# Kernel tuning notes

Measured on AMD Instinct MI355X. Metric: run time of the kernel, lower is better.

The kernel has to match this reference:

```python
import jax, jax.numpy as jnp
import numpy as np

VOCAB = 32000
DIM = 1024
N = 4096
SMOOTHING = 0.1


def setup_inputs() -> dict:
    key = jax.random.key(0)
    kx, kw, ky = jax.random.split(key, 3)
    x = jax.random.normal(kx, (N, DIM), dtype=jnp.float32)
    # xavier_uniform for Linear(dim, vocab): bound = sqrt(6/(dim+vocab))
    bound = float(np.sqrt(6.0 / (DIM + VOCAB)))
    W = jax.random.uniform(kw, (VOCAB, DIM), dtype=jnp.float32, minval=-bound, maxval=bound)
    y = jax.random.randint(ky, (N,), 0, VOCAB, dtype=jnp.int64)
    return {"x": x, "W": W, "y": y}


def reference(x, W, y):
    # logits: [N, V]
    logits = jnp.einsum('nd,vd->nv', x, W)
    log_prb = jax.nn.log_softmax(logits, axis=-1)
    # nll_loss(log_prb, y) with mean reduction
    nll = -jnp.mean(jnp.take_along_axis(log_prb, y[:, None], axis=1)[:, 0])
    # label-smoothed loss: nll*(1-s) - mean(log_prb)*s  (mean over ALL N*V elems)
    loss = nll * (1.0 - SMOOTHING) - jnp.mean(log_prb) * SMOOTHING
    return loss
```

## Files before the change

### kernel.cpp

```cpp
#include <hip/hip_runtime.h>
#include <hip/hip_bf16.h>

#define N_TOK 4096
#define DIM   1024
#define VOCAB 32000
#define BM 128
#define BN 128
#define BKB 128
#define SMOOTH 0.1f

typedef __attribute__((ext_vector_type(4))) float float4v;
typedef __attribute__((ext_vector_type(2))) long long2v;

__global__ void cvt_fp8_2(const float* __restrict__ a, unsigned* __restrict__ da, int n8a,
                          const float* __restrict__ b, unsigned* __restrict__ db, int n8b) {
  int i = blockIdx.x * blockDim.x + threadIdx.x;
  const float4* s; uint2* d; int j; float scl;
  if (i < n8a)            { s = (const float4*)a; d = (uint2*)da; j = i;        scl = 1.f;  }
  else if (i < n8a + n8b) { s = (const float4*)b; d = (uint2*)db; j = i - n8a;  scl = 16.f; }
  else return;
  float4 v0 = s[j * 2], v1 = s[j * 2 + 1];
  unsigned lo = 0, hi = 0;
  lo = __builtin_amdgcn_cvt_pk_fp8_f32(v0.x * scl, v0.y * scl, lo, false);
  lo = __builtin_amdgcn_cvt_pk_fp8_f32(v0.z * scl, v0.w * scl, lo, true);
  hi = __builtin_amdgcn_cvt_pk_fp8_f32(v1.x * scl, v1.y * scl, hi, false);
  hi = __builtin_amdgcn_cvt_pk_fp8_f32(v1.z * scl, v1.w * scl, hi, true);
  uint2 o; o.x = lo; o.y = hi;
  d[j] = o;
}

__device__ __forceinline__ void gload_lds16(const void* g, void* l) {
  __builtin_amdgcn_global_load_lds((const __attribute__((address_space(1))) unsigned int*)g,
                                   (__attribute__((address_space(3))) unsigned int*)l,
                                   16, 0, 0);
}

__global__ __launch_bounds__(256)
void tgt_dot(const float* __restrict__ x, const float* __restrict__ W,
             const int* __restrict__ y, float* __restrict__ tgtRow) {
  const int n = blockIdx.x * 4 + (threadIdx.x >> 6);
  const int lane = threadIdx.x & 63;
  const float4* xr = (const float4*)(x + (size_t)n * DIM);
  const float4* wr = (const float4*)(W + (size_t)y[n] * DIM);
  float d = 0.f;
#pragma unroll
  for (int i = 0; i < 4; ++i) {
    float4 a = xr[lane + 64 * i], b = wr[lane + 64 * i];
    d += a.x * b.x + a.y * b.y + a.z * b.z + a.w * b.w;
  }
#pragma unroll
  for (int off = 32; off > 0; off >>= 1) d += __shfl_xor(d, off, 64);
  if (lane == 0) tgtRow[n] = d;
}

__global__ __launch_bounds__(256, 3)
void gemm_ce(const unsigned char* __restrict__ X8, const unsigned char* __restrict__ W8,
             float* __restrict__ rowExp, float* __restrict__ rowSum) {
  __shared__ __align__(16) unsigned char As[BM * BKB];
  __shared__ __align__(16) unsigned char Bs[BN * BKB];

  const int ib = blockIdx.x;
  const int jb = blockIdx.y;
  const int row0 = ib * BM;
  const int col0 = jb * BN;

  const int tid  = threadIdx.x;
  const int wv   = tid >> 6;
  const int lane = tid & 63;
  const int wr = wv >> 1, wc = wv & 1;
  const int quad = lane >> 4;
  const int r16  = lane & 15;
  const int lrow = lane >> 3;
  const int gcb  = (lane & 7) ^ (lrow & 7);
  const int r8   = r16 & 7;

  float4v acc[4][4];
#pragma unroll
  for (int i = 0; i < 4; ++i)
#pragma unroll
    for (int j = 0; j < 4; ++j) acc[i][j] = (float4v){0.f, 0.f, 0.f, 0.f};

  for (int kk = 0; kk < DIM; kk += BKB) {
    __syncthreads();
#pragma unroll
    for (int c = 0; c < 4; ++c) {
      const int rA = wv * 32 + c * 8;
      gload_lds16(X8 + (size_t)(row0 + rA + lrow) * DIM + kk + gcb * 16, &As[rA * BKB]);
      gload_lds16(W8 + (size_t)(col0 + rA + lrow) * DIM + kk + gcb * 16, &Bs[rA * BKB]);
    }
    __syncthreads();

#pragma unroll
    for (int rr = 0; rr < 2; ++rr) {
      const int cbOff = ((rr * 4 + quad) ^ r8) * 16;
      long2v bf[4];
#pragma unroll
      for (int j = 0; j < 4; ++j)
        bf[j] = *(const long2v*)&Bs[(wc * 64 + j * 16 + r16) * BKB + cbOff];
#pragma unroll
      for (int i = 0; i < 4; ++i) {
        const long2v af = *(const long2v*)&As[(wr * 64 + i * 16 + r16) * BKB + cbOff];
#pragma unroll
        for (int j = 0; j < 4; ++j) {
          acc[i][j] = __builtin_amdgcn_mfma_f32_16x16x32_fp8_fp8(af.x, bf[j].x, acc[i][j], 0, 0, 0);
          acc[i][j] = __builtin_amdgcn_mfma_f32_16x16x32_fp8_fp8(af.y, bf[j].y, acc[i][j], 0, 0, 0);
        }
      }
    }
  }

#pragma unroll
  for (int i = 0; i < 4; ++i)
#pragma unroll
    for (int r = 0; r < 4; ++r) {
      float se = 0.f, ss = 0.f;
#pragma unroll
      for (int j = 0; j < 4; ++j) {
        const float v = acc[i][j][r] * 0.0625f;
        ss += v;
        se += __expf(v);
      }
#pragma unroll
      for (int off = 1; off < 16; off <<= 1) {
        se += __shfl_xor(se, off, 64);
        ss += __shfl_xor(ss, off, 64);
      }
      if (r16 == 0) {
        const int rloc = wr * 64 + i * 16 + quad * 4 + r;
        atomicAdd(&rowExp[row0 + rloc], se);
        atomicAdd(&rowSum[row0 + rloc], ss);
      }
    }
}

__global__ void finalize_kernel(const float* __restrict__ rowExp, const float* __restrict__ rowSum,
                                const float* __restrict__ tgtRow, float* __restrict__ out) {
  __shared__ float s1[256], s2[256], s3[256];
  const int t = threadIdx.x;
  float a = 0.f, b = 0.f, c = 0.f;
  for (int n = t; n < N_TOK; n += 256) {
    a += logf(rowExp[n]);
    b += rowSum[n];
    c += tgtRow[n];
  }
  s1[t] = a; s2[t] = b; s3[t] = c;
  __syncthreads();
  for (int o = 128; o > 0; o >>= 1) {
    if (t < o) { s1[t] += s1[t + o]; s2[t] += s2[t + o]; s3[t] += s3[t + o]; }
    __syncthreads();
  }
  if (t == 0) {
    const float inviN = 1.0f / (float)N_TOK;
    out[0] = s1[0] * inviN
           - (1.0f - SMOOTH) * s3[0] * inviN
           - SMOOTH * s2[0] / ((float)N_TOK * (float)VOCAB);
  }
}

extern "C" void kernel_launch(void* const* d_in, const int* in_sizes, int n_in,
                              void* d_out, int out_size, void* d_ws, size_t ws_size,
                              hipStream_t stream) {
  const float* x = (const float*)d_in[0];
  const float* W = (const float*)d_in[1];
  const int*   y = (const int*)d_in[2];
  float* out = (float*)d_out;

  char* ws = (char*)d_ws;
  float* rowExp = (float*)(ws);
  float* rowSum = (float*)(ws + 16384);
  float* tgtRow = (float*)(ws + 32768);
  unsigned char* X8 = (unsigned char*)(ws + 65536);
  unsigned char* W8 = (unsigned char*)(ws + 65536 + (size_t)N_TOK * DIM);

  hipMemsetAsync(ws, 0, 32768, stream);

  tgt_dot<<<N_TOK / 4, 256, 0, stream>>>(x, W, y, tgtRow);

  const int n8x = N_TOK * DIM / 8, n8w = VOCAB * DIM / 8;
  cvt_fp8_2<<<(n8x + n8w + 255) / 256, 256, 0, stream>>>(x, (unsigned*)X8, n8x, W, (unsigned*)W8, n8w);

  dim3 grid(N_TOK / BM, VOCAB / BN);
  gemm_ce<<<grid, 256, 0, stream>>>(X8, W8, rowExp, rowSum);

  finalize_kernel<<<1, 256, 0, stream>>>(rowExp, rowSum, tgtRow, out);
}
```

Before: 385.8 us.

## Double-buffer LDS tiles with async global-to-LDS prefetch and halved K tile

Switches the fp8 GEMM main loop to two LDS buffers with a K tile of 64 bytes. The next tile is issued via global_load_lds before computing on the current one, gated by manual vmcnt waits and raw s_barrier, so memory latency overlaps MFMA work. The swizzle pattern is adjusted for the narrower rows. Total LDS use stays the same, but each iteration has less MFMA work between barriers, which raises loop and sync overhead. The correctness of the hand-written waitcnt and barrier ordering becomes fragile.

```diff
diff --git a/kernel.cpp b/kernel.cpp
--- a/kernel.cpp
+++ b/kernel.cpp
@@ -6,7 +6,7 @@
 #define VOCAB 32000
 #define BM 128
 #define BN 128
-#define BKB 128
+#define BKB 64
 #define SMOOTH 0.1f
 
 typedef __attribute__((ext_vector_type(4))) float float4v;
@@ -56,8 +56,8 @@
 __global__ __launch_bounds__(256, 3)
 void gemm_ce(const unsigned char* __restrict__ X8, const unsigned char* __restrict__ W8,
              float* __restrict__ rowExp, float* __restrict__ rowSum) {
-  __shared__ __align__(16) unsigned char As[BM * BKB];
-  __shared__ __align__(16) unsigned char Bs[BN * BKB];
+  __shared__ __align__(16) unsigned char As[2][BM * BKB];
+  __shared__ __align__(16) unsigned char Bs[2][BN * BKB];
 
   const int ib = blockIdx.x;
   const int jb = blockIdx.y;
@@ -70,9 +70,19 @@
   const int wr = wv >> 1, wc = wv & 1;
   const int quad = lane >> 4;
   const int r16  = lane & 15;
-  const int lrow = lane >> 3;
-  const int gcb  = (lane & 7) ^ (lrow & 7);
-  const int r8   = r16 & 7;
+  const int lrow4 = lane >> 2;
+  const int gcb4  = (lane & 3) ^ ((lane >> 3) & 3);
+  const int s4    = (r16 >> 1) & 3;
+
+  const unsigned char* pAx = X8 + (size_t)(row0 + wv * 16 + lrow4) * DIM + gcb4 * 16;
+  const unsigned char* pBx = W8 + (size_t)(col0 + wv * 16 + lrow4) * DIM + gcb4 * 16;
+
+#define STAGE(b, kt) do { \
+    gload_lds16(pAx + (kt) * BKB,            &As[b][(wv * 16) * BKB]); \
+    gload_lds16(pAx + 64 * DIM + (kt) * BKB, &As[b][(64 + wv * 16) * BKB]); \
+    gload_lds16(pBx + (kt) * BKB,            &Bs[b][(wv * 16) * BKB]); \
+    gload_lds16(pBx + 64 * DIM + (kt) * BKB, &Bs[b][(64 + wv * 16) * BKB]); \
+  } while (0)
 
   float4v acc[4][4];
 #pragma unroll
@@ -80,33 +90,40 @@
 #pragma unroll
     for (int j = 0; j < 4; ++j) acc[i][j] = (float4v){0.f, 0.f, 0.f, 0.f};
 
-  for (int kk = 0; kk < DIM; kk += BKB) {
-    __syncthreads();
-#pragma unroll
-    for (int c = 0; c < 4; ++c) {
-      const int rA = wv * 32 + c * 8;
-      gload_lds16(X8 + (size_t)(row0 + rA + lrow) * DIM + kk + gcb * 16, &As[rA * BKB]);
-      gload_lds16(W8 + (size_t)(col0 + rA + lrow) * DIM + kk + gcb * 16, &Bs[rA * BKB]);
+  const int cbOff = (quad ^ s4) * 16;
+
+  STAGE(0, 0);
+  int cur = 0;
+
+#pragma unroll 1
+  for (int t = 0; t < DIM / BKB; ++t) {
+    if (t < DIM / BKB - 1) {
+      STAGE(cur ^ 1, t + 1);
+      asm volatile("s_waitcnt vmcnt(4)" ::: "memory");
+    } else {
+      asm volatile("s_waitcnt vmcnt(0)" ::: "memory");
     }
-    __syncthreads();
-
-#pragma unroll
-    for (int rr = 0; rr < 2; ++rr) {
-      const int cbOff = ((rr * 4 + quad) ^ r8) * 16;
-      long2v bf[4];
-#pragma unroll
-      for (int j = 0; j < 4; ++j)
-        bf[j] = *(const long2v*)&Bs[(wc * 64 + j * 16 + r16) * BKB + cbOff];
-#pragma unroll
-      for (int i = 0; i < 4; ++i) {
-        const long2v af = *(const long2v*)&As[(wr * 64 + i * 16 + r16) * BKB + cbOff];
-#pragma unroll
-        for (int j = 0; j < 4; ++j) {
-          acc[i][j] = __builtin_amdgcn_mfma_f32_16x16x32_fp8_fp8(af.x, bf[j].x, acc[i][j], 0, 0, 0);
-          acc[i][j] = __builtin_amdgcn_mfma_f32_16x16x32_fp8_fp8(af.y, bf[j].y, acc[i][j], 0, 0, 0);
-        }
+    __builtin_amdgcn_s_barrier();
+    __builtin_amdgcn_sched_barrier(0);
+
+    long2v bf[4];
+#pragma unroll
+    for (int j = 0; j < 4; ++j)
+      bf[j] = *(const long2v*)&Bs[cur][(wc * 64 + j * 16 + r16) * BKB + cbOff];
+#pragma unroll
+    for (int i = 0; i < 4; ++i) {
+      const long2v af = *(const long2v*)&As[cur][(wr * 64 + i * 16 + r16) * BKB + cbOff];
+#pragma unroll
+      for (int j = 0; j < 4; ++j) {
+        acc[i][j] = __builtin_amdgcn_mfma_f32_16x16x32_fp8_fp8(af.x, bf[j].x, acc[i][j], 0, 0, 0);
+        acc[i][j] = __builtin_amdgcn_mfma_f32_16x16x32_fp8_fp8(af.y, bf[j].y, acc[i][j], 0, 0, 0);
       }
     }
+
+    asm volatile("" ::: "memory");
+    __builtin_amdgcn_s_barrier();
+    asm volatile("" ::: "memory");
+    cur ^= 1;
   }
 
 #pragma unroll
```

Measured after the change: 413.6 us. 1.07x slower.
